# Kernel optimization log

Hardware: AMD Instinct MI355X
Metric: run time of the kernel (lower is better)

The kernel has to match this reference:

```python
import jax, jax.numpy as jnp
import numpy as np

CUTOFFS = [16000, 28000, 36000]
HID = 1024
PROJ = [256, 64]  # hidden/4**1, hidden/4**2 per compute_proj_dims
CLUSTERS = 2


def setup_inputs() -> dict:
    key = jax.random.key(0)
    ks = jax.random.split(key, 12)
    B, S = 4, 1024
    scale = 0.02
    d = {
        "inp": jax.random.normal(ks[0], (B, S, HID), jnp.float32),
        "labels": jax.random.randint(ks[1], (B, S), 0, CUTOFFS[-1]),
        "head_W": jax.random.normal(ks[2], (HID, CUTOFFS[0] + CLUSTERS), jnp.float32) * scale,
        "head_b": jnp.zeros((CUTOFFS[0] + CLUSTERS,), jnp.float32),
    }
    for i in range(CLUSTERS):
        tdim = CUTOFFS[i + 1] - CUTOFFS[i]
        d[f"t{i}_pW"] = jax.random.normal(ks[3 + 4 * i], (HID, PROJ[i]), jnp.float32) * scale
        d[f"t{i}_pb"] = jnp.zeros((PROJ[i],), jnp.float32)
        d[f"t{i}_W"] = jax.random.normal(ks[4 + 4 * i], (PROJ[i], CUTOFFS[i + 1] - CUTOFFS[i]), jnp.float32) * scale
        d[f"t{i}_b"] = jnp.zeros((CUTOFFS[i + 1] - CUTOFFS[i],), jnp.float32)
    return d


def _sparse_ce(logits, labels):
    # stable sparse softmax cross entropy, single log_softmax pass
    logp = jax.nn.log_softmax(logits, axis=-1)
    return -jnp.take_along_axis(logp, labels[..., None], axis=-1)[..., 0]


def reference(inp, labels, head_W, head_b, t0_pW, t0_pb, t0_W, t0_b, t1_pW, t1_pb, t1_W, t1_b):
    tails = [(t0_pW, t0_pb, t0_W, t0_b), (t1_pW, t1_pb, t1_W, t1_b)]
    head_labels = labels
    loss = jnp.zeros(labels.shape, inp.dtype)
    for i, (pW, pb, W, b) in enumerate(tails):
        lo, hi = CUTOFFS[i], CUTOFFS[i + 1]
        mask = (labels >= lo) & (labels < hi)
        # tokens in cluster i are relabeled to cluster id in the head
        head_labels = jnp.where(mask, CUTOFFS[0] + i, head_labels)
        # two-layer tail projection: [B,S,H] -> [B,S,proj] -> [B,S,tail_dim]
        tail_logits = (inp @ pW + pb) @ W + b
        tail_labels = jnp.clip(labels - lo, 0, hi - lo - 1)
        loss = loss + jnp.where(mask, _sparse_ce(tail_logits, tail_labels), 0.0)
    head_logits = inp @ head_W + head_b  # [B,S,cutoffs[0]+clusters]
    loss = _sparse_ce(head_logits, head_labels) + loss
    loss = loss * (labels != 0).astype(loss.dtype)  # zero out pad positions
    return jnp.mean(loss)
```

## Files before the change

kernel.cpp:

```cpp
#include <hip/hip_runtime.h>
#include <hip/hip_bf16.h>
#include <cstdint>
#include <cstddef>

#define M_TOK 4096
#define HID   1024
#define NHEAD 16002
#define NHEAD_PAD 16128
#define P0    256
#define N0    12000
#define N0_PAD 12032
#define P1    64
#define N1    8000
#define N1_PAD 8192
#define PFUSE 384
#define PREAL 320

typedef unsigned char u8;
typedef float f32x4 __attribute__((ext_vector_type(4)));
typedef int   i32x4 __attribute__((ext_vector_type(4)));
typedef int   i32x8 __attribute__((ext_vector_type(8)));

__device__ __forceinline__ void load16(const void* g, void* l) {
    __builtin_amdgcn_global_load_lds(
        (__attribute__((address_space(1))) void*)g,
        (__attribute__((address_space(3))) void*)l,
        16, 0, 0);
}

__device__ __forceinline__ u8 to_e4m3(float f) {
    return (u8)(__builtin_amdgcn_cvt_pk_fp8_f32(f, f, 0, false) & 0xff);
}
__device__ __forceinline__ unsigned cvt4(float x, float y, float z, float w) {
    int r = __builtin_amdgcn_cvt_pk_fp8_f32(x, y, 0, false);
    r = __builtin_amdgcn_cvt_pk_fp8_f32(z, w, r, true);
    return (unsigned)r;
}

union Frag { struct { i32x4 lo, hi; } half; i32x8 v; };

struct Seg {
    const u8* A; int lda;
    const u8* BT; int ldb;
    const float* bias; int K; int realN;
    const int* tgt; float* sumexp; float* lab;
    int nblk;
};

__launch_bounds__(512, 4)
__global__ void gemm_lse3(Seg s0, Seg s1, Seg s2) {
    __shared__ __align__(16) u8 As[32768];
    __shared__ __align__(16) u8 Bs[16384];

    int b = blockIdx.x;
    Seg sg; int rel;
    if (b < s0.nblk)                { sg = s0; rel = b; }
    else if (b < s0.nblk + s1.nblk) { sg = s1; rel = b - s0.nblk; }
    else                            { sg = s2; rel = b - s0.nblk - s1.nblk; }
    int pair = rel >> 5, inner = rel & 31;
    int m0 = (inner >> 1) * 256;
    int n0 = (pair * 2 + (inner & 1)) * 128;

    const int lda = sg.lda, ldb = sg.ldb;
    const int tid  = threadIdx.x;
    const int lane = tid & 63;
    const int wave = tid >> 6;
    const int wm = wave >> 1, wn = wave & 1;
    const int q = lane >> 4, lrow = lane & 15;
    const int sw = lrow & 7;

    int aofs[4], abase[4], bofs[2], bbase[2];
    #pragma unroll
    for (int p = 0; p < 4; p++) {
        int pg = wave * 256 + p * 64 + lane;
        int row = pg >> 3, gcol = (pg & 7) ^ (row & 7);
        aofs[p]  = row * lda + gcol * 16;
        abase[p] = (wave * 256 + p * 64) * 16;
    }
    #pragma unroll
    for (int p = 0; p < 2; p++) {
        int pg = wave * 128 + p * 64 + lane;
        int row = pg >> 3, gcol = (pg & 7) ^ (row & 7);
        bofs[p]  = row * ldb + gcol * 16;
        bbase[p] = (wave * 128 + p * 64) * 16;
    }

    f32x4 acc[4][4];
    #pragma unroll
    for (int mt = 0; mt < 4; mt++)
        #pragma unroll
        for (int nt = 0; nt < 4; nt++)
            acc[mt][nt] = (f32x4)(0.0f);

    const u8* Ab = sg.A  + (size_t)m0 * lda;
    const u8* Bb = sg.BT + (size_t)n0 * ldb;

    const int aLo = ((wm * 64 + lrow) * 8 + ((2 * q)     ^ sw)) * 16;
    const int aHi = ((wm * 64 + lrow) * 8 + ((2 * q + 1) ^ sw)) * 16;
    const int bLo = ((wn * 64 + lrow) * 8 + ((2 * q)     ^ sw)) * 16;
    const int bHi = ((wn * 64 + lrow) * 8 + ((2 * q + 1) ^ sw)) * 16;

    for (int k0 = 0; k0 < sg.K; k0 += 128) {
        #pragma unroll
        for (int p = 0; p < 4; p++)
            load16(Ab + k0 + aofs[p], As + abase[p]);
        #pragma unroll
        for (int p = 0; p < 2; p++)
            load16(Bb + k0 + bofs[p], Bs + bbase[p]);
        __syncthreads();

        Frag fb[4];
        #pragma unroll
        for (int t = 0; t < 4; t++) {
            fb[t].half.lo = *reinterpret_cast<const i32x4*>(Bs + bLo + t * 2048);
            fb[t].half.hi = *reinterpret_cast<const i32x4*>(Bs + bHi + t * 2048);
        }
        Frag fa[2];
        fa[0].half.lo = *reinterpret_cast<const i32x4*>(As + aLo);
        fa[0].half.hi = *reinterpret_cast<const i32x4*>(As + aHi);
        #pragma unroll
        for (int mt = 0; mt < 4; mt++) {
            if (mt < 3) {
                fa[(mt + 1) & 1].half.lo = *reinterpret_cast<const i32x4*>(As + aLo + (mt + 1) * 2048);
                fa[(mt + 1) & 1].half.hi = *reinterpret_cast<const i32x4*>(As + aHi + (mt + 1) * 2048);
            }
            #pragma unroll
            for (int nt = 0; nt < 4; nt++)
                acc[mt][nt] = __builtin_amdgcn_mfma_scale_f32_16x16x128_f8f6f4(
                    fa[mt & 1].v, fb[nt].v, acc[mt][nt],
                    0, 0,
                    0, 0x7F7F7F7F,
                    0, 0x7A7A7A7A);
        }
        __syncthreads();
    }

    int colg[4]; float bias_v[4];
    #pragma unroll
    for (int nt = 0; nt < 4; nt++) {
        colg[nt] = n0 + wn * 64 + nt * 16 + lrow;
        bias_v[nt] = (colg[nt] < sg.realN) ? sg.bias[colg[nt]] : 0.0f;
    }

    float* sred = reinterpret_cast<float*>(As);

    #pragma unroll
    for (int mt = 0; mt < 4; mt++) {
        int rloc = wm * 64 + mt * 16 + q * 4;
        #pragma unroll
        for (int r = 0; r < 4; r++) {
            int tok = m0 + rloc + r;
            int tg = sg.tgt[tok];
            float ps = 0.0f;
            #pragma unroll
            for (int nt = 0; nt < 4; nt++) {
                if (colg[nt] < sg.realN) {
                    float logit = acc[mt][nt][r] + bias_v[nt];
                    ps += __expf(logit);
                    if (colg[nt] == tg) atomicAdd(&sg.lab[tok], logit);
                }
            }
            ps += __shfl_xor(ps, 1);
            ps += __shfl_xor(ps, 2);
            ps += __shfl_xor(ps, 4);
            ps += __shfl_xor(ps, 8);
            if (lrow == 0) sred[wn * 256 + rloc + r] = ps;
        }
    }
    __syncthreads();
    if (tid < 256) {
        float v = sred[tid] + sred[256 + tid];
        atomicAdd(&sg.sumexp[m0 + tid], v);
    }
}

__device__ __forceinline__ void proj_body(const u8* __restrict__ A, const u8* __restrict__ BT,
                                          const float* __restrict__ bias, u8* __restrict__ out,
                                          int m0, int n0, u8* As, u8* Bs) {
    const int lda = HID, ldb = HID, ldo = PFUSE;
    const int tid  = threadIdx.x;
    const int lane = tid & 63;
    const int wave = tid >> 6;
    const int wm = wave >> 2, wn = wave & 3;
    const int q = lane >> 4, lrow = lane & 15;
    const int sw = lrow & 7;

    int aofs[2], bofs[2], lbase[2];
    #pragma unroll
    for (int p = 0; p < 2; p++) {
        int pg = wave * 128 + p * 64 + lane;
        int row = pg >> 3, gcol = (pg & 7) ^ (row & 7);
        aofs[p]  = row * lda + gcol * 16;
        bofs[p]  = row * ldb + gcol * 16;
        lbase[p] = (wave * 128 + p * 64) * 16;
    }

    f32x4 acc[4][2];
    #pragma unroll
    for (int mt = 0; mt < 4; mt++)
        #pragma unroll
        for (int nt = 0; nt < 2; nt++)
            acc[mt][nt] = (f32x4)(0.0f);

    const u8* Ab = A  + (size_t)m0 * lda;
    const u8* Bb = BT + (size_t)n0 * ldb;

    const int aLo = ((wm * 64 + lrow) * 8 + ((2 * q)     ^ sw)) * 16;
    const int aHi = ((wm * 64 + lrow) * 8 + ((2 * q + 1) ^ sw)) * 16;
    const int bLo = ((wn * 32 + lrow) * 8 + ((2 * q)     ^ sw)) * 16;
    const int bHi = ((wn * 32 + lrow) * 8 + ((2 * q + 1) ^ sw)) * 16;

    for (int k0 = 0; k0 < HID; k0 += 128) {
        #pragma unroll
        for (int p = 0; p < 2; p++) {
            load16(Ab + k0 + aofs[p], As + lbase[p]);
            load16(Bb + k0 + bofs[p], Bs + lbase[p]);
        }
        __syncthreads();
        Frag fb[2];
        #pragma unroll
        for (int t = 0; t < 2; t++) {
            fb[t].half.lo = *reinterpret_cast<const i32x4*>(Bs + bLo + t * 2048);
            fb[t].half.hi = *reinterpret_cast<const i32x4*>(Bs + bHi + t * 2048);
        }
        #pragma unroll
        for (int mt = 0; mt < 4; mt++) {
            Frag fa;
            fa.half.lo = *reinterpret_cast<const i32x4*>(As + aLo + mt * 2048);
            fa.half.hi = *reinterpret_cast<const i32x4*>(As + aHi + mt * 2048);
            #pragma unroll
            for (int nt = 0; nt < 2; nt++)
                acc[mt][nt] = __builtin_amdgcn_mfma_scale_f32_16x16x128_f8f6f4(
                    fa.v, fb[nt].v, acc[mt][nt],
                    0, 0, 0, 0x7F7F7F7F, 0, 0x7A7A7A7A);
        }
        __syncthreads();
    }

    int colg[2]; float bias_v[2];
    #pragma unroll
    for (int nt = 0; nt < 2; nt++) {
        colg[nt] = n0 + wn * 32 + nt * 16 + lrow;
        bias_v[nt] = (colg[nt] < PREAL) ? bias[colg[nt]] : 0.0f;
    }
    #pragma unroll
    for (int mt = 0; mt < 4; mt++) {
        int rowb = m0 + wm * 64 + mt * 16 + q * 4;
        #pragma unroll
        for (int r = 0; r < 4; r++) {
            int tok = rowb + r;
            #pragma unroll
            for (int nt = 0; nt < 2; nt++)
                out[(size_t)tok * ldo + colg[nt]] = to_e4m3(acc[mt][nt][r] + bias_v[nt]);
        }
    }
}

__device__ __forceinline__ void tr_cast(const float* __restrict__ W, u8* __restrict__ WT,
                                        int K, int N, int Kpad, float scale,
                                        int bx, int by, u8* ldsb ) {
    int n0 = bx * 64, k0 = by * 128;
    int c4 = threadIdx.x & 15;
    int rg = threadIdx.x >> 4;
    int n = n0 + c4 * 4;
    #pragma unroll
    for (int j = 0; j < 4; j++) {
        int kr = rg + j * 32;
        int k = k0 + kr;
        float2 v01 = make_float2(0.f, 0.f), v23 = make_float2(0.f, 0.f);
        if (k < K) {
            const float* row = W + (size_t)k * N;
            if (n + 3 < N) {
                v01 = *reinterpret_cast<const float2*>(row + n);
                v23 = *reinterpret_cast<const float2*>(row + n + 2);
            } else {
                if (n     < N) v01.x = row[n];
                if (n + 1 < N) v01.y = row[n + 1];
                if (n + 2 < N) v23.x = row[n + 2];
                if (n + 3 < N) v23.y = row[n + 3];
            }
        }
        unsigned pk = cvt4(v01.x * scale, v01.y * scale, v23.x * scale, v23.y * scale);
        *reinterpret_cast<unsigned*>(ldsb + kr * 68 + c4 * 4) = pk;
    }
    __syncthreads();
    int nn = threadIdx.x >> 3, kb = (threadIdx.x & 7) * 16;
    union { u8 b[16]; uint4 u; } o;
    #pragma unroll
    for (int j = 0; j < 16; j++) o.b[j] = ldsb[(kb + j) * 68 + nn];
    *reinterpret_cast<uint4*>(WT + (size_t)(n0 + nn) * Kpad + k0 + kb) = o.u;
}

#define P1_CAST 256
#define P1_T0P   32
#define P1_T1P   16
#define P1_INIT   8

__global__ void prep1_kernel(const float* __restrict__ inp, const int* __restrict__ labels,
                             const float* __restrict__ t0_pW, const float* __restrict__ t0_pb,
                             const float* __restrict__ t1_pW, const float* __restrict__ t1_pb,
                             u8* __restrict__ inp_f8, u8* __restrict__ fpW8,
                             float* __restrict__ acc6, int* __restrict__ tgts,
                             float* __restrict__ pbias, float* __restrict__ out) {
    __shared__ __align__(16) u8 ldsb[128 * 68];
    int b = blockIdx.x;
    if (b < P1_CAST) {
        #pragma unroll
        for (int h = 0; h < 2; h++) {
            int i = b * 1024 + h * 512 + threadIdx.x;
            float4 v = reinterpret_cast<const float4*>(inp)[i];
            reinterpret_cast<unsigned*>(inp_f8)[i] = cvt4(v.x, v.y, v.z, v.w);
        }
    } else if (b < P1_CAST + P1_T0P) {
        int r = b - P1_CAST;
        tr_cast(t0_pW, fpW8, HID, P0, HID, 32.0f, r & 3, r >> 2, ldsb);
    } else if (b < P1_CAST + P1_T0P + P1_T1P) {
        int r = b - (P1_CAST + P1_T0P);
        tr_cast(t1_pW, fpW8 + 256 * HID, HID, P1, HID, 32.0f, r & 1, r >> 1, ldsb);
    } else {
        int r = b - (P1_CAST + P1_T0P + P1_T1P);
        int t = r * 512 + threadIdx.x;
        for (int j = t; j < 6 * M_TOK; j += M_TOK) acc6[j] = 0.0f;
        if (t == 0) out[0] = 0.0f;
        if (t < PFUSE) pbias[t] = (t < 256) ? t0_pb[t] : ((t < PREAL) ? t1_pb[t - 256] : 0.0f);
        int lbl = labels[t];
        tgts[t]             = (lbl < 16000) ? lbl : ((lbl < 28000) ? 16000 : 16001);
        int t0 = lbl - 16000; t0 = t0 < 0 ? 0 : (t0 > 11999 ? 11999 : t0);
        int t1 = lbl - 28000; t1 = t1 < 0 ? 0 : (t1 > 7999  ? 7999  : t1);
        tgts[M_TOK + t]     = t0;
        tgts[2 * M_TOK + t] = t1;
    }
}

#define P2_HEAD 2016
#define P2_T0W   376
#define P2_T1W   128
#define P2_PROJ   96

__launch_bounds__(512, 4)
__global__ void prep2_kernel(const float* __restrict__ head_W,
                             const float* __restrict__ t0_W, const float* __restrict__ t1_W,
                             const u8* __restrict__ inp_f8, const u8* __restrict__ fpW8,
                             const float* __restrict__ pbias,
                             u8* __restrict__ headW8, u8* __restrict__ t0W8,
                             u8* __restrict__ t1W8, u8* __restrict__ proj8) {
    __shared__ __align__(16) u8 smem[32768];
    int b = blockIdx.x;
    if (b < P2_HEAD) {
        tr_cast(head_W, headW8, HID, NHEAD, HID, 32.0f, b % 252, b / 252, smem);
    } else if (b < P2_HEAD + P2_T0W) {
        int r = b - P2_HEAD;
        tr_cast(t0_W, t0W8, P0, N0, P0, 32.0f, r % 188, r / 188, smem);
    } else if (b < P2_HEAD + P2_T0W + P2_T1W) {
        int r = b - (P2_HEAD + P2_T0W);
        tr_cast(t1_W, t1W8, P1, N1, 128, 32.0f, r, 0, smem);
    } else {
        int r = b - (P2_HEAD + P2_T0W + P2_T1W);
        int m0 = (r & 31) * 128;
        int n0 = (r >> 5) * 128;
        proj_body(inp_f8, fpW8, pbias, proj8, m0, n0, smem, smem + 16384);
    }
}

__global__ void finalize_kernel(const int* __restrict__ labels, const float* __restrict__ acc6,
                                float* __restrict__ out) {
    int t = blockIdx.x * blockDim.x + threadIdx.x;
    const float* sumH = acc6;
    const float* labH = acc6 + M_TOK;
    const float* sum0 = acc6 + 2 * M_TOK;
    const float* lab0 = acc6 + 3 * M_TOK;
    const float* sum1 = acc6 + 4 * M_TOK;
    const float* lab1 = acc6 + 5 * M_TOK;
    int lbl = labels[t];
    float l = 0.0f;
    if (lbl != 0) {
        l = logf(sumH[t]) - labH[t];
        if (lbl >= 16000 && lbl < 28000) l += logf(sum0[t]) - lab0[t];
        else if (lbl >= 28000)           l += logf(sum1[t]) - lab1[t];
    }
    l *= (1.0f / (float)M_TOK);
    #pragma unroll
    for (int off = 1; off < 64; off <<= 1) l += __shfl_xor(l, off);
    __shared__ float red[4];
    if ((threadIdx.x & 63) == 0) red[threadIdx.x >> 6] = l;
    __syncthreads();
    if (threadIdx.x == 0) atomicAdd(out, red[0] + red[1] + red[2] + red[3]);
}

extern "C" void kernel_launch(void* const* d_in, const int* in_sizes, int n_in,
                              void* d_out, int out_size, void* d_ws, size_t ws_size,
                              hipStream_t stream) {
    const float* inp    = (const float*)d_in[0];
    const int*   labels = (const int*)  d_in[1];
    const float* head_W = (const float*)d_in[2];
    const float* head_b = (const float*)d_in[3];
    const float* t0_pW  = (const float*)d_in[4];
    const float* t0_pb  = (const float*)d_in[5];
    const float* t0_W   = (const float*)d_in[6];
    const float* t0_b   = (const float*)d_in[7];
    const float* t1_pW  = (const float*)d_in[8];
    const float* t1_pb  = (const float*)d_in[9];
    const float* t1_W   = (const float*)d_in[10];
    const float* t1_b   = (const float*)d_in[11];
    float* out = (float*)d_out;

    char* ws = (char*)d_ws;
    size_t off = 0;
    auto alloc = [&](size_t bytes) { char* p = ws + off; off += (bytes + 255) & ~(size_t)255; return p; };
    u8*    inp_f8  = (u8*)   alloc((size_t)M_TOK * HID);
    u8*    headW8  = (u8*)   alloc((size_t)NHEAD_PAD * HID);
    u8*    fpW8    = (u8*)   alloc((size_t)PFUSE * HID);
    u8*    t0W8    = (u8*)   alloc((size_t)N0_PAD * P0);
    u8*    t1W8    = (u8*)   alloc((size_t)N1_PAD * 128);
    u8*    proj8   = (u8*)   alloc((size_t)M_TOK * PFUSE);
    float* acc6    = (float*)alloc(6 * M_TOK * 4);
    int*   tgts    = (int*)  alloc(3 * M_TOK * 4);
    float* pbias   = (float*)alloc(PFUSE * 4);

    prep1_kernel<<<P1_CAST + P1_T0P + P1_T1P + P1_INIT, 512, 0, stream>>>(
        inp, labels, t0_pW, t0_pb, t1_pW, t1_pb,
        inp_f8, fpW8, acc6, tgts, pbias, out);

    prep2_kernel<<<P2_HEAD + P2_T0W + P2_T1W + P2_PROJ, 512, 0, stream>>>(
        head_W, t0_W, t1_W, inp_f8, fpW8, pbias,
        headW8, t0W8, t1W8, proj8);

    Seg s0{inp_f8,      HID,   headW8, HID, head_b, HID, NHEAD, tgts,             acc6,             acc6 + M_TOK,     16 * (NHEAD_PAD / 128)};
    Seg s1{proj8,       PFUSE, t0W8,   P0,  t0_b,   P0,  N0,    tgts + M_TOK,     acc6 + 2 * M_TOK, acc6 + 3 * M_TOK, 16 * (N0_PAD / 128)};
    Seg s2{proj8 + 256, PFUSE, t1W8,   128, t1_b,   128, N1,    tgts + 2 * M_TOK, acc6 + 4 * M_TOK, acc6 + 5 * M_TOK, 16 * (N1_PAD / 128)};
    gemm_lse3<<<s0.nblk + s1.nblk + s2.nblk, 512, 0, stream>>>(s0, s1, s2);

    finalize_kernel<<<M_TOK / 256, 256, 0, stream>>>(labels, acc6, out);
}
```

Before: 289.8 us.

## Merge prep kernels by fusing fp8 casts into projection GEMM and remap tile order

Collapses the two preparation kernels into one launch. The projection GEMM now reads fp32 inputs and projection weights directly, casting them to fp8 into shared memory, which removes the dependency on a prior cast kernel and the separate transposed projection-weight buffer. The main GEMM's block-to-tile mapping is changed to an interleaved order across 8 groups, intended to improve cache locality across concurrently scheduled blocks. The cost is that projection blocks do scalar strided fp32 loads and duplicate input conversion work, and the reordering may hurt L2 reuse if the grouping assumption is wrong.

```diff
diff --git a/kernel.cpp b/kernel.cpp
--- a/kernel.cpp
+++ b/kernel.cpp
@@ -57,9 +57,10 @@
     if (b < s0.nblk)                { sg = s0; rel = b; }
     else if (b < s0.nblk + s1.nblk) { sg = s1; rel = b - s0.nblk; }
     else                            { sg = s2; rel = b - s0.nblk - s1.nblk; }
-    int pair = rel >> 5, inner = rel & 31;
-    int m0 = (inner >> 1) * 256;
-    int n0 = (pair * 2 + (inner & 1)) * 128;
+    int chunk = sg.nblk >> 3;
+    int L = (rel & 7) * chunk + (rel >> 3);
+    int m0 = (L & 15) * 256;
+    int n0 = (L >> 4) * 128;
 
     const int lda = sg.lda, ldb = sg.ldb;
     const int tid  = threadIdx.x;
@@ -174,10 +175,13 @@
     }
 }
 
-__device__ __forceinline__ void proj_body(const u8* __restrict__ A, const u8* __restrict__ BT,
-                                          const float* __restrict__ bias, u8* __restrict__ out,
-                                          int m0, int n0, u8* As, u8* Bs) {
-    const int lda = HID, ldb = HID, ldo = PFUSE;
+__device__ __forceinline__ void proj_inline(const float* __restrict__ inp,
+                                            const float* __restrict__ t0_pW,
+                                            const float* __restrict__ t0_pb,
+                                            const float* __restrict__ t1_pW,
+                                            const float* __restrict__ t1_pb,
+                                            u8* __restrict__ out,
+                                            int m0, int n0, u8* As, u8* Bs) {
     const int tid  = threadIdx.x;
     const int lane = tid & 63;
     const int wave = tid >> 6;
@@ -185,15 +189,19 @@
     const int q = lane >> 4, lrow = lane & 15;
     const int sw = lrow & 7;
 
-    int aofs[2], bofs[2], lbase[2];
-    #pragma unroll
-    for (int p = 0; p < 2; p++) {
-        int pg = wave * 128 + p * 64 + lane;
-        int row = pg >> 3, gcol = (pg & 7) ^ (row & 7);
-        aofs[p]  = row * lda + gcol * 16;
-        bofs[p]  = row * ldb + gcol * 16;
-        lbase[p] = (wave * 128 + p * 64) * 16;
-    }
+    const float* Wb; int NW, nreal;
+    if (n0 < 256) { Wb = t0_pW + n0; NW = P0; nreal = 128; }
+    else          { Wb = t1_pW;      NW = P1; nreal = 64;  }
+
+    const int ar  = tid >> 2;
+    const int ag0 = (tid & 3) * 2;
+    const float* Arow = inp + (size_t)(m0 + ar) * HID;
+    u8* AsW0 = As + ar * 128 + ((ag0    ) ^ (ar & 7)) * 16;
+    u8* AsW1 = As + ar * 128 + ((ag0 + 1) ^ (ar & 7)) * 16;
+
+    const int bn  = tid & 127;
+    const int kq0 = (tid >> 7) * 8;
+    const bool breal = bn < nreal;
 
     f32x4 acc[4][2];
     #pragma unroll
@@ -201,22 +209,37 @@
         #pragma unroll
         for (int nt = 0; nt < 2; nt++)
             acc[mt][nt] = (f32x4)(0.0f);
-
-    const u8* Ab = A  + (size_t)m0 * lda;
-    const u8* Bb = BT + (size_t)n0 * ldb;
 
     const int aLo = ((wm * 64 + lrow) * 8 + ((2 * q)     ^ sw)) * 16;
     const int aHi = ((wm * 64 + lrow) * 8 + ((2 * q + 1) ^ sw)) * 16;
     const int bLo = ((wn * 32 + lrow) * 8 + ((2 * q)     ^ sw)) * 16;
     const int bHi = ((wn * 32 + lrow) * 8 + ((2 * q + 1) ^ sw)) * 16;
 
-    for (int k0 = 0; k0 < HID; k0 += 128) {
-        #pragma unroll
-        for (int p = 0; p < 2; p++) {
-            load16(Ab + k0 + aofs[p], As + lbase[p]);
-            load16(Bb + k0 + bofs[p], Bs + lbase[p]);
+    for (int ks = 0; ks < 8; ks++) {
+        const int k0 = ks * 128;
+        unsigned aw[8];
+        #pragma unroll
+        for (int g = 0; g < 2; g++)
+            #pragma unroll
+            for (int j = 0; j < 4; j++) {
+                float4 v = *reinterpret_cast<const float4*>(Arow + k0 + (ag0 + g) * 16 + j * 4);
+                aw[g * 4 + j] = cvt4(v.x, v.y, v.z, v.w);
+            }
+        *reinterpret_cast<uint4*>(AsW0) = make_uint4(aw[0], aw[1], aw[2], aw[3]);
+        *reinterpret_cast<uint4*>(AsW1) = make_uint4(aw[4], aw[5], aw[6], aw[7]);
+        #pragma unroll
+        for (int i = 0; i < 8; i++) {
+            int kq = kq0 + i;
+            float f0 = 0.f, f1 = 0.f, f2 = 0.f, f3 = 0.f;
+            if (breal) {
+                const float* p = Wb + (size_t)(k0 + kq * 4) * NW + bn;
+                f0 = p[0]; f1 = p[NW]; f2 = p[2 * NW]; f3 = p[3 * NW];
+            }
+            unsigned pk = cvt4(f0 * 32.f, f1 * 32.f, f2 * 32.f, f3 * 32.f);
+            *reinterpret_cast<unsigned*>(Bs + bn * 128 + ((kq >> 2) ^ (bn & 7)) * 16 + (kq & 3) * 4) = pk;
         }
         __syncthreads();
+
         Frag fb[2];
         #pragma unroll
         for (int t = 0; t < 2; t++) {
@@ -241,7 +264,8 @@
     #pragma unroll
     for (int nt = 0; nt < 2; nt++) {
         colg[nt] = n0 + wn * 32 + nt * 16 + lrow;
-        bias_v[nt] = (colg[nt] < PREAL) ? bias[colg[nt]] : 0.0f;
+        bias_v[nt] = (colg[nt] < 256) ? t0_pb[colg[nt]]
+                   : ((colg[nt] < PREAL) ? t1_pb[colg[nt] - 256] : 0.0f);
     }
     #pragma unroll
     for (int mt = 0; mt < 4; mt++) {
@@ -251,7 +275,7 @@
             int tok = rowb + r;
             #pragma unroll
             for (int nt = 0; nt < 2; nt++)
-                out[(size_t)tok * ldo + colg[nt]] = to_e4m3(acc[mt][nt][r] + bias_v[nt]);
+                out[(size_t)tok * PFUSE + colg[nt]] = to_e4m3(acc[mt][nt][r] + bias_v[nt]);
         }
     }
 }
@@ -291,74 +315,59 @@
     *reinterpret_cast<uint4*>(WT + (size_t)(n0 + nn) * Kpad + k0 + kb) = o.u;
 }
 
-#define P1_CAST 256
-#define P1_T0P   32
-#define P1_T1P   16
-#define P1_INIT   8
-
-__global__ void prep1_kernel(const float* __restrict__ inp, const int* __restrict__ labels,
-                             const float* __restrict__ t0_pW, const float* __restrict__ t0_pb,
-                             const float* __restrict__ t1_pW, const float* __restrict__ t1_pb,
-                             u8* __restrict__ inp_f8, u8* __restrict__ fpW8,
-                             float* __restrict__ acc6, int* __restrict__ tgts,
-                             float* __restrict__ pbias, float* __restrict__ out) {
-    __shared__ __align__(16) u8 ldsb[128 * 68];
+#define PB_PROJ   96
+#define PB_HEAD 2016
+#define PB_T0W   376
+#define PB_T1W   128
+#define PB_CAST  256
+#define PB_INIT    8
+
+__launch_bounds__(512, 4)
+__global__ void prep_kernel(const float* __restrict__ inp, const int* __restrict__ labels,
+                            const float* __restrict__ head_W,
+                            const float* __restrict__ t0_pW, const float* __restrict__ t0_pb,
+                            const float* __restrict__ t0_W,
+                            const float* __restrict__ t1_pW, const float* __restrict__ t1_pb,
+                            const float* __restrict__ t1_W,
+                            u8* __restrict__ inp_f8, u8* __restrict__ headW8,
+                            u8* __restrict__ t0W8, u8* __restrict__ t1W8,
+                            u8* __restrict__ proj8,
+                            float* __restrict__ acc6, int* __restrict__ tgts,
+                            float* __restrict__ out) {
+    __shared__ __align__(16) u8 smem[32768];
     int b = blockIdx.x;
-    if (b < P1_CAST) {
+    if (b < PB_PROJ) {
+        int m0 = (b % 32) * 128;
+        int n0 = (b / 32) * 128;
+        proj_inline(inp, t0_pW, t0_pb, t1_pW, t1_pb, proj8, m0, n0, smem, smem + 16384);
+    } else if (b < PB_PROJ + PB_HEAD) {
+        int r = b - PB_PROJ;
+        tr_cast(head_W, headW8, HID, NHEAD, HID, 32.0f, r % 252, r / 252, smem);
+    } else if (b < PB_PROJ + PB_HEAD + PB_T0W) {
+        int r = b - (PB_PROJ + PB_HEAD);
+        tr_cast(t0_W, t0W8, P0, N0, P0, 32.0f, r % 188, r / 188, smem);
+    } else if (b < PB_PROJ + PB_HEAD + PB_T0W + PB_T1W) {
+        int r = b - (PB_PROJ + PB_HEAD + PB_T0W);
+        tr_cast(t1_W, t1W8, P1, N1, 128, 32.0f, r, 0, smem);
+    } else if (b < PB_PROJ + PB_HEAD + PB_T0W + PB_T1W + PB_CAST) {
+        int r = b - (PB_PROJ + PB_HEAD + PB_T0W + PB_T1W);
         #pragma unroll
         for (int h = 0; h < 2; h++) {
-            int i = b * 1024 + h * 512 + threadIdx.x;
+            int i = r * 1024 + h * 512 + threadIdx.x;
             float4 v = reinterpret_cast<const float4*>(inp)[i];
             reinterpret_cast<unsigned*>(inp_f8)[i] = cvt4(v.x, v.y, v.z, v.w);
         }
-    } else if (b < P1_CAST + P1_T0P) {
-        int r = b - P1_CAST;
-        tr_cast(t0_pW, fpW8, HID, P0, HID, 32.0f, r & 3, r >> 2, ldsb);
-    } else if (b < P1_CAST + P1_T0P + P1_T1P) {
-        int r = b - (P1_CAST + P1_T0P);
-        tr_cast(t1_pW, fpW8 + 256 * HID, HID, P1, HID, 32.0f, r & 1, r >> 1, ldsb);
     } else {
-        int r = b - (P1_CAST + P1_T0P + P1_T1P);
+        int r = b - (PB_PROJ + PB_HEAD + PB_T0W + PB_T1W + PB_CAST);
         int t = r * 512 + threadIdx.x;
         for (int j = t; j < 6 * M_TOK; j += M_TOK) acc6[j] = 0.0f;
         if (t == 0) out[0] = 0.0f;
-        if (t < PFUSE) pbias[t] = (t < 256) ? t0_pb[t] : ((t < PREAL) ? t1_pb[t - 256] : 0.0f);
         int lbl = labels[t];
         tgts[t]             = (lbl < 16000) ? lbl : ((lbl < 28000) ? 16000 : 16001);
         int t0 = lbl - 16000; t0 = t0 < 0 ? 0 : (t0 > 11999 ? 11999 : t0);
         int t1 = lbl - 28000; t1 = t1 < 0 ? 0 : (t1 > 7999  ? 7999  : t1);
         tgts[M_TOK + t]     = t0;
         tgts[2 * M_TOK + t] = t1;
-    }
-}
-
-#define P2_HEAD 2016
-#define P2_T0W   376
-#define P2_T1W   128
-#define P2_PROJ   96
-
-__launch_bounds__(512, 4)
-__global__ void prep2_kernel(const float* __restrict__ head_W,
-                             const float* __restrict__ t0_W, const float* __restrict__ t1_W,
-                             const u8* __restrict__ inp_f8, const u8* __restrict__ fpW8,
-                             const float* __restrict__ pbias,
-                             u8* __restrict__ headW8, u8* __restrict__ t0W8,
-                             u8* __restrict__ t1W8, u8* __restrict__ proj8) {
-    __shared__ __align__(16) u8 smem[32768];
-    int b = blockIdx.x;
-    if (b < P2_HEAD) {
-        tr_cast(head_W, headW8, HID, NHEAD, HID, 32.0f, b % 252, b / 252, smem);
-    } else if (b < P2_HEAD + P2_T0W) {
-        int r = b - P2_HEAD;
-        tr_cast(t0_W, t0W8, P0, N0, P0, 32.0f, r % 188, r / 188, smem);
-    } else if (b < P2_HEAD + P2_T0W + P2_T1W) {
-        int r = b - (P2_HEAD + P2_T0W);
-        tr_cast(t1_W, t1W8, P1, N1, 128, 32.0f, r, 0, smem);
-    } else {
-        int r = b - (P2_HEAD + P2_T0W + P2_T1W);
-        int m0 = (r & 31) * 128;
-        int n0 = (r >> 5) * 128;
-        proj_body(inp_f8, fpW8, pbias, proj8, m0, n0, smem, smem + 16384);
     }
 }
 
@@ -409,21 +418,15 @@
     auto alloc = [&](size_t bytes) { char* p = ws + off; off += (bytes + 255) & ~(size_t)255; return p; };
     u8*    inp_f8  = (u8*)   alloc((size_t)M_TOK * HID);
     u8*    headW8  = (u8*)   alloc((size_t)NHEAD_PAD * HID);
-    u8*    fpW8    = (u8*)   alloc((size_t)PFUSE * HID);
     u8*    t0W8    = (u8*)   alloc((size_t)N0_PAD * P0);
     u8*    t1W8    = (u8*)   alloc((size_t)N1_PAD * 128);
     u8*    proj8   = (u8*)   alloc((size_t)M_TOK * PFUSE);
     float* acc6    = (float*)alloc(6 * M_TOK * 4);
     int*   tgts    = (int*)  alloc(3 * M_TOK * 4);
-    float* pbias   = (float*)alloc(PFUSE * 4);
-
-    prep1_kernel<<<P1_CAST + P1_T0P + P1_T1P + P1_INIT, 512, 0, stream>>>(
-        inp, labels, t0_pW, t0_pb, t1_pW, t1_pb,
-        inp_f8, fpW8, acc6, tgts, pbias, out);
-
-    prep2_kernel<<<P2_HEAD + P2_T0W + P2_T1W + P2_PROJ, 512, 0, stream>>>(
-        head_W, t0_W, t1_W, inp_f8, fpW8, pbias,
-        headW8, t0W8, t1W8, proj8);
+
+    prep_kernel<<<PB_PROJ + PB_HEAD + PB_T0W + PB_T1W + PB_CAST + PB_INIT, 512, 0, stream>>>(
+        inp, labels, head_W, t0_pW, t0_pb, t0_W, t1_pW, t1_pb, t1_W,
+        inp_f8, headW8, t0W8, t1W8, proj8, acc6, tgts, out);
 
     Seg s0{inp_f8,      HID,   headW8, HID, head_b, HID, NHEAD, tgts,             acc6,             acc6 + M_TOK,     16 * (NHEAD_PAD / 128)};
     Seg s1{proj8,       PFUSE, t0W8,   P0,  t0_b,   P0,  N0,    tgts + M_TOK,     acc6 + 2 * M_TOK, acc6 + 3 * M_TOK, 16 * (N0_PAD / 128)};
```

Result: no change. 294.2 us (+1.5%).
